# Kernel optimization log

Measured on AMD Instinct MI355X. Metric: run time of the kernel, lower is better.

## Reference

```python
import jax, jax.numpy as jnp
import numpy as np

N = 50000   # nodes
E = 800000  # edges
H = 128     # hidden dim
V = 50000   # feats_per_node (embedding vocab)


def setup_inputs() -> dict:
    key = jax.random.key(0)
    ks = jax.random.split(key, 16)
    s = 0.05  # keep activations in a sane range
    return {
        "node_ids": jax.random.randint(ks[0], (N,), 0, V),
        "src": jax.random.randint(ks[1], (E,), 0, N),
        "dst": jnp.sort(jax.random.randint(ks[2], (E,), 0, N)),
        "emb": jax.random.normal(ks[3], (V, H), jnp.float32) * s,
        "W_pool1": jax.random.normal(ks[4], (H, H), jnp.float32) * s,
        "b_pool1": jax.random.normal(ks[5], (H,), jnp.float32) * s,
        "W_self1": jax.random.normal(ks[6], (H, H), jnp.float32) * s,
        "W_neigh1": jax.random.normal(ks[7], (H, H), jnp.float32) * s,
        "b1": jax.random.normal(ks[8], (H,), jnp.float32) * s,
        "W_pool2": jax.random.normal(ks[9], (H, H), jnp.float32) * s,
        "b_pool2": jax.random.normal(ks[10], (H,), jnp.float32) * s,
        "W_self2": jax.random.normal(ks[11], (H, H), jnp.float32) * s,
        "W_neigh2": jax.random.normal(ks[12], (H, H), jnp.float32) * s,
        "b2": jax.random.normal(ks[13], (H,), jnp.float32) * s,
    }


def _sage_pool_layer(h, src, dst, W_pool, b_pool, W_self, W_neigh, b):
    # DGL SAGEConv('pool'): per-src MLP, gather over edges, segmented max per dst.
    m = jax.nn.relu(h @ W_pool + b_pool)              # [N, H]
    msgs = m[src]                                     # [E, H] gather
    agg = jax.ops.segment_max(msgs, dst, num_segments=N,
                              indices_are_sorted=True)  # [N, H]
    agg = jnp.where(jnp.isneginf(agg), 0.0, agg)      # zero-in-degree -> 0 (DGL semantics)
    return h @ W_self + agg @ W_neigh + b


def reference(node_ids, src, dst, emb,
              W_pool1, b_pool1, W_self1, W_neigh1, b1,
              W_pool2, b_pool2, W_self2, W_neigh2, b2):
    h = emb[node_ids]                                 # embedding_h on 1-hot indices
    h = _sage_pool_layer(h, src, dst, W_pool1, b_pool1, W_self1, W_neigh1, b1)
    h = _sage_pool_layer(h, src, dst, W_pool2, b_pool2, W_self2, W_neigh2, b2)
    return h
```

## Files before the change

kernel.cpp:

```cpp
#include <hip/hip_runtime.h>

#define HD 128

typedef __attribute__((ext_vector_type(8))) short short8;
typedef __attribute__((ext_vector_type(4))) float floatx4;

typedef unsigned short ushort_t;
typedef unsigned int uint_t;

__device__ __forceinline__ ushort_t f2b(float f) {
    union { float f; uint_t u; } v; v.f = f;
    uint_t r = v.u + 0x7fff + ((v.u >> 16) & 1);
    return (ushort_t)(r >> 16);
}
__device__ __forceinline__ float b_lo(uint_t p) {
    union { uint_t u; float f; } v; v.u = p << 16; return v.f;
}
__device__ __forceinline__ float b_hi(uint_t p) {
    union { uint_t u; float f; } v; v.u = p & 0xffff0000u; return v.f;
}
__device__ __forceinline__ uint_t packb(float a, float b) {
    union { float f; uint_t u; } x, y; x.f = a; y.f = b;
    return (x.u >> 16) | (y.u & 0xffff0000u);
}

__global__ __launch_bounds__(256) void k_rowptr(const int* __restrict__ dst, int E,
                                                int* __restrict__ rp, int N) {
    int i = blockIdx.x * blockDim.x + threadIdx.x;
    if (i > N) return;
    int lo = 0, hi = E;
    while (lo < hi) {
        int mid = (lo + hi) >> 1;
        if (dst[mid] < i) lo = mid + 1; else hi = mid;
    }
    rp[i] = lo;
}

__global__ __launch_bounds__(256) void k_gather(const int* __restrict__ ids,
                                                const float* __restrict__ emb,
                                                ushort_t* __restrict__ h, int N) {
    int idx = blockIdx.x * blockDim.x + threadIdx.x;
    int row = idx >> 5;
    if (row >= N) return;
    int c = (idx & 31) * 4;
    float4 v = *(const float4*)&emb[(size_t)ids[row] * HD + c];
    uint_t o0 = packb(b_lo(0), 0.f);
    (void)o0;
    uint2 o;
    o.x = (uint_t)f2b(v.x) | ((uint_t)f2b(v.y) << 16);
    o.y = (uint_t)f2b(v.z) | ((uint_t)f2b(v.w) << 16);
    *(uint2*)&h[(size_t)row * HD + c] = o;
}

__global__ __launch_bounds__(256) void k_pack(const float* W0, const float* W1,
                                              const float* W2, const float* W3,
                                              const float* W4, const float* W5,
                                              ushort_t* __restrict__ out) {
    const float* Ws[6] = {W0, W1, W2, W3, W4, W5};
    int mat = blockIdx.x >> 6;
    int o = ((blockIdx.x & 63) << 8) + threadIdx.x;
    int j = o & 7, l = (o >> 3) & 63, s = (o >> 9) & 3, t = o >> 11;
    int k = s * 32 + ((l >> 4) & 3) * 8 + j;
    int n = t * 16 + (l & 15);
    out[(size_t)mat * 16384 + o] = f2b(Ws[mat][k * HD + n]);
}

__global__ __launch_bounds__(256) void k_pool_mfma(const ushort_t* __restrict__ h,
                                                   const ushort_t* __restrict__ Wpk,
                                                   const float* __restrict__ bias,
                                                   ushort_t* __restrict__ m, int N) {
    int wave = blockIdx.x * 4 + (threadIdx.x >> 6);
    int row0 = wave * 16;
    if (row0 >= N) return;
    int l = threadIdx.x & 63;
    int ar = row0 + (l & 15);
    if (ar >= N) ar = N - 1;
    int ac = (l >> 4) * 8;
    short8 a[4];
#pragma unroll
    for (int s = 0; s < 4; ++s)
        a[s] = *(const short8*)&h[(size_t)ar * HD + s * 32 + ac];

    int rbase = row0 + (l >> 4) * 4;
#pragma unroll
    for (int t = 0; t < 8; ++t) {
        floatx4 acc = {0.f, 0.f, 0.f, 0.f};
#pragma unroll
        for (int s = 0; s < 4; ++s) {
            short8 b = *(const short8*)&Wpk[(t * 4 + s) * 512 + l * 8];
            acc = __builtin_amdgcn_mfma_f32_16x16x32_bf16(a[s], b, acc, 0, 0, 0);
        }
        int col = t * 16 + (l & 15);
        float bv = bias[col];
#pragma unroll
        for (int r = 0; r < 4; ++r) {
            int gr = rbase + r;
            if (gr < N)
                m[(size_t)gr * HD + col] = f2b(fmaxf(acc[r] + bv, 0.f));
        }
    }
}

template <bool F32OUT>
__global__ __launch_bounds__(256) void k_dual_mfma(const ushort_t* __restrict__ h,
                                                   const ushort_t* __restrict__ agg,
                                                   const ushort_t* __restrict__ WsPk,
                                                   const ushort_t* __restrict__ WnPk,
                                                   const float* __restrict__ bias,
                                                   void* __restrict__ outp, int N) {
    int wave = blockIdx.x * 4 + (threadIdx.x >> 6);
    int row0 = wave * 16;
    if (row0 >= N) return;
    int l = threadIdx.x & 63;
    int ar = row0 + (l & 15);
    if (ar >= N) ar = N - 1;
    int ac = (l >> 4) * 8;
    short8 ah[4], ag[4];
#pragma unroll
    for (int s = 0; s < 4; ++s) {
        ah[s] = *(const short8*)&h[(size_t)ar * HD + s * 32 + ac];
        ag[s] = *(const short8*)&agg[(size_t)ar * HD + s * 32 + ac];
    }

    int rbase = row0 + (l >> 4) * 4;
#pragma unroll
    for (int t = 0; t < 8; ++t) {
        floatx4 acc = {0.f, 0.f, 0.f, 0.f};
#pragma unroll
        for (int s = 0; s < 4; ++s) {
            short8 bs = *(const short8*)&WsPk[(t * 4 + s) * 512 + l * 8];
            acc = __builtin_amdgcn_mfma_f32_16x16x32_bf16(ah[s], bs, acc, 0, 0, 0);
        }
#pragma unroll
        for (int s = 0; s < 4; ++s) {
            short8 bn = *(const short8*)&WnPk[(t * 4 + s) * 512 + l * 8];
            acc = __builtin_amdgcn_mfma_f32_16x16x32_bf16(ag[s], bn, acc, 0, 0, 0);
        }
        int col = t * 16 + (l & 15);
        float bv = bias[col];
#pragma unroll
        for (int r = 0; r < 4; ++r) {
            int gr = rbase + r;
            if (gr < N) {
                float v = acc[r] + bv;
                if (F32OUT) ((float*)outp)[(size_t)gr * HD + col] = v;
                else        ((ushort_t*)outp)[(size_t)gr * HD + col] = f2b(v);
            }
        }
    }
}

__global__ __launch_bounds__(256) void k_segmax(const ushort_t* __restrict__ m,
                                                const int* __restrict__ src,
                                                const int* __restrict__ rp,
                                                ushort_t* __restrict__ agg, int N) {
    int node = blockIdx.x * 8 + (threadIdx.x >> 5);
    if (node >= N) return;
    int lane = threadIdx.x & 31;
    int beg = rp[node], end = rp[node + 1];
    float a0 = 0.f, a1 = 0.f, a2 = 0.f, a3 = 0.f;
    float c0 = 0.f, c1 = 0.f, c2 = 0.f, c3 = 0.f;
    int e = beg;
    for (; e + 2 <= end; e += 2) {
        int s0 = src[e], s1 = src[e + 1];
        uint2 p = *(const uint2*)&m[(size_t)s0 * HD + lane * 4];
        uint2 q = *(const uint2*)&m[(size_t)s1 * HD + lane * 4];
        a0 = fmaxf(a0, b_lo(p.x)); a1 = fmaxf(a1, b_hi(p.x));
        a2 = fmaxf(a2, b_lo(p.y)); a3 = fmaxf(a3, b_hi(p.y));
        c0 = fmaxf(c0, b_lo(q.x)); c1 = fmaxf(c1, b_hi(q.x));
        c2 = fmaxf(c2, b_lo(q.y)); c3 = fmaxf(c3, b_hi(q.y));
    }
    if (e < end) {
        uint2 p = *(const uint2*)&m[(size_t)src[e] * HD + lane * 4];
        a0 = fmaxf(a0, b_lo(p.x)); a1 = fmaxf(a1, b_hi(p.x));
        a2 = fmaxf(a2, b_lo(p.y)); a3 = fmaxf(a3, b_hi(p.y));
    }
    a0 = fmaxf(a0, c0); a1 = fmaxf(a1, c1); a2 = fmaxf(a2, c2); a3 = fmaxf(a3, c3);
    uint2 o; o.x = packb(a0, a1); o.y = packb(a2, a3);
    *(uint2*)&agg[(size_t)node * HD + lane * 4] = o;
}

extern "C" void kernel_launch(void* const* d_in, const int* in_sizes, int n_in,
                              void* d_out, int out_size, void* d_ws, size_t ws_size,
                              hipStream_t stream) {
    const int*   node_ids = (const int*)d_in[0];
    const int*   src      = (const int*)d_in[1];
    const int*   dst      = (const int*)d_in[2];
    const float* emb      = (const float*)d_in[3];
    const float* Wp1      = (const float*)d_in[4];
    const float* bp1      = (const float*)d_in[5];
    const float* Ws1      = (const float*)d_in[6];
    const float* Wn1      = (const float*)d_in[7];
    const float* b1       = (const float*)d_in[8];
    const float* Wp2      = (const float*)d_in[9];
    const float* bp2      = (const float*)d_in[10];
    const float* Ws2      = (const float*)d_in[11];
    const float* Wn2      = (const float*)d_in[12];
    const float* b2       = (const float*)d_in[13];
    float* out = (float*)d_out;

    const int N = in_sizes[0];
    const int E = in_sizes[1];

    char* ws = (char*)d_ws;
    int* rp = (int*)ws;
    size_t off = (((size_t)(N + 1) * 4) + 255) & ~(size_t)255;
    ushort_t* Wpk  = (ushort_t*)(ws + off);
    ushort_t* h0   = Wpk + 6 * 16384;
    ushort_t* bufM = h0 + (size_t)N * HD;
    ushort_t* bufA = bufM + (size_t)N * HD;
    ushort_t* h1   = bufA + (size_t)N * HD;

    const int nb_gemm = (N / 16 + 3) / 4;
    const int nb_seg  = (N + 7) / 8;

    k_rowptr<<<(N + 256) / 256, 256, 0, stream>>>(dst, E, rp, N);
    k_gather<<<(N * 32 + 255) / 256, 256, 0, stream>>>(node_ids, emb, h0, N);
    k_pack<<<6 * 64, 256, 0, stream>>>(Wp1, Ws1, Wn1, Wp2, Ws2, Wn2, Wpk);

    const ushort_t* Wp1k = Wpk;
    const ushort_t* Ws1k = Wpk + 16384;
    const ushort_t* Wn1k = Wpk + 2 * 16384;
    const ushort_t* Wp2k = Wpk + 3 * 16384;
    const ushort_t* Ws2k = Wpk + 4 * 16384;
    const ushort_t* Wn2k = Wpk + 5 * 16384;

    k_pool_mfma<<<nb_gemm, 256, 0, stream>>>(h0, Wp1k, bp1, bufM, N);
    k_segmax<<<nb_seg, 256, 0, stream>>>(bufM, src, rp, bufA, N);
    k_dual_mfma<false><<<nb_gemm, 256, 0, stream>>>(h0, bufA, Ws1k, Wn1k, b1, h1, N);

    k_pool_mfma<<<nb_gemm, 256, 0, stream>>>(h1, Wp2k, bp2, bufM, N);
    k_segmax<<<nb_seg, 256, 0, stream>>>(bufM, src, rp, bufA, N);
    k_dual_mfma<true><<<nb_gemm, 256, 0, stream>>>(h1, bufA, Ws2k, Wn2k, b2, out, N);
}
```

Baseline: 250.7 us.

## Merge prep kernels, process 32 rows per wave in GEMMs, unroll segmax by four

Fuses the row-pointer search, embedding gather and weight packing into one launch to cut two kernel launches. The pool and dual GEMM kernels now compute two 16-row tiles per wave, reusing each loaded weight fragment for two MFMAs and halving the grid. The segment-max loop is unrolled to four edges per iteration for more memory-level parallelism. The larger per-wave tiles raise register use, and the smaller grid may leave fewer waves available to hide latency.

```diff
diff --git a/kernel.cpp b/kernel.cpp
--- a/kernel.cpp
+++ b/kernel.cpp
@@ -24,45 +24,46 @@
     return (x.u >> 16) | (y.u & 0xffff0000u);
 }
 
-__global__ __launch_bounds__(256) void k_rowptr(const int* __restrict__ dst, int E,
-                                                int* __restrict__ rp, int N) {
-    int i = blockIdx.x * blockDim.x + threadIdx.x;
-    if (i > N) return;
-    int lo = 0, hi = E;
-    while (lo < hi) {
-        int mid = (lo + hi) >> 1;
-        if (dst[mid] < i) lo = mid + 1; else hi = mid;
-    }
-    rp[i] = lo;
-}
-
-__global__ __launch_bounds__(256) void k_gather(const int* __restrict__ ids,
-                                                const float* __restrict__ emb,
-                                                ushort_t* __restrict__ h, int N) {
-    int idx = blockIdx.x * blockDim.x + threadIdx.x;
-    int row = idx >> 5;
-    if (row >= N) return;
-    int c = (idx & 31) * 4;
-    float4 v = *(const float4*)&emb[(size_t)ids[row] * HD + c];
-    uint_t o0 = packb(b_lo(0), 0.f);
-    (void)o0;
-    uint2 o;
-    o.x = (uint_t)f2b(v.x) | ((uint_t)f2b(v.y) << 16);
-    o.y = (uint_t)f2b(v.z) | ((uint_t)f2b(v.w) << 16);
-    *(uint2*)&h[(size_t)row * HD + c] = o;
-}
-
-__global__ __launch_bounds__(256) void k_pack(const float* W0, const float* W1,
+__global__ __launch_bounds__(256) void k_prep(const int* __restrict__ dst, int E,
+                                              int* __restrict__ rp, int N,
+                                              const int* __restrict__ ids,
+                                              const float* __restrict__ emb,
+                                              ushort_t* __restrict__ h0,
+                                              const float* W0, const float* W1,
                                               const float* W2, const float* W3,
                                               const float* W4, const float* W5,
-                                              ushort_t* __restrict__ out) {
-    const float* Ws[6] = {W0, W1, W2, W3, W4, W5};
-    int mat = blockIdx.x >> 6;
-    int o = ((blockIdx.x & 63) << 8) + threadIdx.x;
-    int j = o & 7, l = (o >> 3) & 63, s = (o >> 9) & 3, t = o >> 11;
-    int k = s * 32 + ((l >> 4) & 3) * 8 + j;
-    int n = t * 16 + (l & 15);
-    out[(size_t)mat * 16384 + o] = f2b(Ws[mat][k * HD + n]);
+                                              ushort_t* __restrict__ Wpk,
+                                              int nbG, int nbR) {
+    int b = blockIdx.x;
+    if (b < nbG) {
+        int idx = b * 256 + threadIdx.x;
+        int row = idx >> 5;
+        if (row >= N) return;
+        int c = (idx & 31) * 4;
+        float4 v = *(const float4*)&emb[(size_t)ids[row] * HD + c];
+        uint2 o;
+        o.x = (uint_t)f2b(v.x) | ((uint_t)f2b(v.y) << 16);
+        o.y = (uint_t)f2b(v.z) | ((uint_t)f2b(v.w) << 16);
+        *(uint2*)&h0[(size_t)row * HD + c] = o;
+    } else if (b < nbG + nbR) {
+        int i = (b - nbG) * 256 + threadIdx.x;
+        if (i > N) return;
+        int lo = 0, hi = E;
+        while (lo < hi) {
+            int mid = (lo + hi) >> 1;
+            if (dst[mid] < i) lo = mid + 1; else hi = mid;
+        }
+        rp[i] = lo;
+    } else {
+        int bb = b - nbG - nbR;
+        const float* Ws[6] = {W0, W1, W2, W3, W4, W5};
+        int mat = bb >> 6;
+        int o = ((bb & 63) << 8) + threadIdx.x;
+        int j = o & 7, l = (o >> 3) & 63, s = (o >> 9) & 3, t = o >> 11;
+        int k = s * 32 + ((l >> 4) & 3) * 8 + j;
+        int n = t * 16 + (l & 15);
+        Wpk[(size_t)mat * 16384 + o] = f2b(Ws[mat][k * HD + n]);
+    }
 }
 
 __global__ __launch_bounds__(256) void k_pool_mfma(const ushort_t* __restrict__ h,
@@ -70,33 +71,36 @@
                                                    const float* __restrict__ bias,
                                                    ushort_t* __restrict__ m, int N) {
     int wave = blockIdx.x * 4 + (threadIdx.x >> 6);
-    int row0 = wave * 16;
+    int row0 = wave * 32;
     if (row0 >= N) return;
     int l = threadIdx.x & 63;
-    int ar = row0 + (l & 15);
-    if (ar >= N) ar = N - 1;
+    int ar0 = row0 + (l & 15); if (ar0 >= N) ar0 = N - 1;
+    int ar1 = ar0 + 16;        if (ar1 >= N) ar1 = N - 1;
     int ac = (l >> 4) * 8;
-    short8 a[4];
-#pragma unroll
-    for (int s = 0; s < 4; ++s)
-        a[s] = *(const short8*)&h[(size_t)ar * HD + s * 32 + ac];
-
-    int rbase = row0 + (l >> 4) * 4;
+    short8 a0[4], a1[4];
+#pragma unroll
+    for (int s = 0; s < 4; ++s) {
+        a0[s] = *(const short8*)&h[(size_t)ar0 * HD + s * 32 + ac];
+        a1[s] = *(const short8*)&h[(size_t)ar1 * HD + s * 32 + ac];
+    }
+    int rb = row0 + (l >> 4) * 4;
 #pragma unroll
     for (int t = 0; t < 8; ++t) {
-        floatx4 acc = {0.f, 0.f, 0.f, 0.f};
+        floatx4 acc0 = {0.f, 0.f, 0.f, 0.f};
+        floatx4 acc1 = {0.f, 0.f, 0.f, 0.f};
 #pragma unroll
         for (int s = 0; s < 4; ++s) {
             short8 b = *(const short8*)&Wpk[(t * 4 + s) * 512 + l * 8];
-            acc = __builtin_amdgcn_mfma_f32_16x16x32_bf16(a[s], b, acc, 0, 0, 0);
+            acc0 = __builtin_amdgcn_mfma_f32_16x16x32_bf16(a0[s], b, acc0, 0, 0, 0);
+            acc1 = __builtin_amdgcn_mfma_f32_16x16x32_bf16(a1[s], b, acc1, 0, 0, 0);
         }
         int col = t * 16 + (l & 15);
         float bv = bias[col];
 #pragma unroll
         for (int r = 0; r < 4; ++r) {
-            int gr = rbase + r;
-            if (gr < N)
-                m[(size_t)gr * HD + col] = f2b(fmaxf(acc[r] + bv, 0.f));
+            int g0 = rb + r, g1 = rb + 16 + r;
+            if (g0 < N) m[(size_t)g0 * HD + col] = f2b(fmaxf(acc0[r] + bv, 0.f));
+            if (g1 < N) m[(size_t)g1 * HD + col] = f2b(fmaxf(acc1[r] + bv, 0.f));
         }
     }
 }
@@ -109,42 +113,49 @@
                                                    const float* __restrict__ bias,
                                                    void* __restrict__ outp, int N) {
     int wave = blockIdx.x * 4 + (threadIdx.x >> 6);
-    int row0 = wave * 16;
+    int row0 = wave * 32;
     if (row0 >= N) return;
     int l = threadIdx.x & 63;
-    int ar = row0 + (l & 15);
-    if (ar >= N) ar = N - 1;
+    int ar0 = row0 + (l & 15); if (ar0 >= N) ar0 = N - 1;
+    int ar1 = ar0 + 16;        if (ar1 >= N) ar1 = N - 1;
     int ac = (l >> 4) * 8;
-    short8 ah[4], ag[4];
+    short8 ah0[4], ah1[4], ag0[4], ag1[4];
 #pragma unroll
     for (int s = 0; s < 4; ++s) {
-        ah[s] = *(const short8*)&h[(size_t)ar * HD + s * 32 + ac];
-        ag[s] = *(const short8*)&agg[(size_t)ar * HD + s * 32 + ac];
-    }
-
-    int rbase = row0 + (l >> 4) * 4;
+        ah0[s] = *(const short8*)&h[(size_t)ar0 * HD + s * 32 + ac];
+        ah1[s] = *(const short8*)&h[(size_t)ar1 * HD + s * 32 + ac];
+        ag0[s] = *(const short8*)&agg[(size_t)ar0 * HD + s * 32 + ac];
+        ag1[s] = *(const short8*)&agg[(size_t)ar1 * HD + s * 32 + ac];
+    }
+    int rb = row0 + (l >> 4) * 4;
 #pragma unroll
     for (int t = 0; t < 8; ++t) {
-        floatx4 acc = {0.f, 0.f, 0.f, 0.f};
+        floatx4 acc0 = {0.f, 0.f, 0.f, 0.f};
+        floatx4 acc1 = {0.f, 0.f, 0.f, 0.f};
 #pragma unroll
         for (int s = 0; s < 4; ++s) {
             short8 bs = *(const short8*)&WsPk[(t * 4 + s) * 512 + l * 8];
-            acc = __builtin_amdgcn_mfma_f32_16x16x32_bf16(ah[s], bs, acc, 0, 0, 0);
+            acc0 = __builtin_amdgcn_mfma_f32_16x16x32_bf16(ah0[s], bs, acc0, 0, 0, 0);
+            acc1 = __builtin_amdgcn_mfma_f32_16x16x32_bf16(ah1[s], bs, acc1, 0, 0, 0);
         }
 #pragma unroll
         for (int s = 0; s < 4; ++s) {
             short8 bn = *(const short8*)&WnPk[(t * 4 + s) * 512 + l * 8];
-            acc = __builtin_amdgcn_mfma_f32_16x16x32_bf16(ag[s], bn, acc, 0, 0, 0);
+            acc0 = __builtin_amdgcn_mfma_f32_16x16x32_bf16(ag0[s], bn, acc0, 0, 0, 0);
+            acc1 = __builtin_amdgcn_mfma_f32_16x16x32_bf16(ag1[s], bn, acc1, 0, 0, 0);
         }
         int col = t * 16 + (l & 15);
         float bv = bias[col];
 #pragma unroll
         for (int r = 0; r < 4; ++r) {
-            int gr = rbase + r;
-            if (gr < N) {
-                float v = acc[r] + bv;
-                if (F32OUT) ((float*)outp)[(size_t)gr * HD + col] = v;
-                else        ((ushort_t*)outp)[(size_t)gr * HD + col] = f2b(v);
+            int g0 = rb + r, g1 = rb + 16 + r;
+            float v0 = acc0[r] + bv, v1 = acc1[r] + bv;
+            if (F32OUT) {
+                if (g0 < N) ((float*)outp)[(size_t)g0 * HD + col] = v0;
+                if (g1 < N) ((float*)outp)[(size_t)g1 * HD + col] = v1;
+            } else {
+                if (g0 < N) ((ushort_t*)outp)[(size_t)g0 * HD + col] = f2b(v0);
+                if (g1 < N) ((ushort_t*)outp)[(size_t)g1 * HD + col] = f2b(v1);
             }
         }
     }
@@ -161,16 +172,23 @@
     float a0 = 0.f, a1 = 0.f, a2 = 0.f, a3 = 0.f;
     float c0 = 0.f, c1 = 0.f, c2 = 0.f, c3 = 0.f;
     int e = beg;
-    for (; e + 2 <= end; e += 2) {
-        int s0 = src[e], s1 = src[e + 1];
-        uint2 p = *(const uint2*)&m[(size_t)s0 * HD + lane * 4];
-        uint2 q = *(const uint2*)&m[(size_t)s1 * HD + lane * 4];
-        a0 = fmaxf(a0, b_lo(p.x)); a1 = fmaxf(a1, b_hi(p.x));
-        a2 = fmaxf(a2, b_lo(p.y)); a3 = fmaxf(a3, b_hi(p.y));
-        c0 = fmaxf(c0, b_lo(q.x)); c1 = fmaxf(c1, b_hi(q.x));
-        c2 = fmaxf(c2, b_lo(q.y)); c3 = fmaxf(c3, b_hi(q.y));
-    }
-    if (e < end) {
+    int e4 = beg + ((end - beg) & ~3);
+    for (; e < e4; e += 4) {
+        int s0 = src[e], s1 = src[e + 1], s2 = src[e + 2], s3 = src[e + 3];
+        uint2 p0 = *(const uint2*)&m[(size_t)s0 * HD + lane * 4];
+        uint2 p1 = *(const uint2*)&m[(size_t)s1 * HD + lane * 4];
+        uint2 p2 = *(const uint2*)&m[(size_t)s2 * HD + lane * 4];
+        uint2 p3 = *(const uint2*)&m[(size_t)s3 * HD + lane * 4];
+        a0 = fmaxf(a0, b_lo(p0.x)); a1 = fmaxf(a1, b_hi(p0.x));
+        a2 = fmaxf(a2, b_lo(p0.y)); a3 = fmaxf(a3, b_hi(p0.y));
+        c0 = fmaxf(c0, b_lo(p1.x)); c1 = fmaxf(c1, b_hi(p1.x));
+        c2 = fmaxf(c2, b_lo(p1.y)); c3 = fmaxf(c3, b_hi(p1.y));
+        a0 = fmaxf(a0, b_lo(p2.x)); a1 = fmaxf(a1, b_hi(p2.x));
+        a2 = fmaxf(a2, b_lo(p2.y)); a3 = fmaxf(a3, b_hi(p2.y));
+        c0 = fmaxf(c0, b_lo(p3.x)); c1 = fmaxf(c1, b_hi(p3.x));
+        c2 = fmaxf(c2, b_lo(p3.y)); c3 = fmaxf(c3, b_hi(p3.y));
+    }
+    for (; e < end; ++e) {
         uint2 p = *(const uint2*)&m[(size_t)src[e] * HD + lane * 4];
         a0 = fmaxf(a0, b_lo(p.x)); a1 = fmaxf(a1, b_hi(p.x));
         a2 = fmaxf(a2, b_lo(p.y)); a3 = fmaxf(a3, b_hi(p.y));
@@ -211,12 +229,15 @@
     ushort_t* bufA = bufM + (size_t)N * HD;
     ushort_t* h1   = bufA + (size_t)N * HD;
 
-    const int nb_gemm = (N / 16 + 3) / 4;
+    const int nbG = (N * 32 + 255) / 256;
+    const int nbR = (N + 1 + 255) / 256;
+    const int nbP = 6 * 64;
+    const int nb_gemm = (N + 127) / 128;
     const int nb_seg  = (N + 7) / 8;
 
-    k_rowptr<<<(N + 256) / 256, 256, 0, stream>>>(dst, E, rp, N);
-    k_gather<<<(N * 32 + 255) / 256, 256, 0, stream>>>(node_ids, emb, h0, N);
-    k_pack<<<6 * 64, 256, 0, stream>>>(Wp1, Ws1, Wn1, Wp2, Ws2, Wn2, Wpk);
+    k_prep<<<nbG + nbR + nbP, 256, 0, stream>>>(dst, E, rp, N, node_ids, emb, h0,
+                                                Wp1, Ws1, Wn1, Wp2, Ws2, Wn2, Wpk,
+                                                nbG, nbR);
 
     const ushort_t* Wp1k = Wpk;
     const ushort_t* Ws1k = Wpk + 16384;
```

New measurement: 245.9 us. Within noise of the previous version (-1.9%).
